# Kernel optimization log

Hardware: AMD Instinct MI355X
Metric: run time of the kernel (lower is better)

## Reference

```python
import jax, jax.numpy as jnp
import numpy as np

N_NODES = 50000
N_EDGES = 800000
DIM_IN = 128
DIM_OUT = 64


def setup_inputs() -> dict:
    key = jax.random.key(0)
    k1, k2, k3, k4 = jax.random.split(key, 4)
    x = jax.random.normal(k1, (N_NODES, DIM_IN), dtype=jnp.float32)
    edge_index = jax.random.randint(k2, (2, N_EDGES), 0, N_NODES, dtype=jnp.int64)
    W = jax.random.normal(k3, (DIM_IN, DIM_OUT), dtype=jnp.float32) / np.sqrt(DIM_IN)
    b = jax.random.normal(k4, (DIM_OUT,), dtype=jnp.float32) * 0.01
    return {"x": x, "edge_index": edge_index, "W": W, "b": b}


def reference(x, edge_index, W, b):
    # Faithful PyG GCNConv: add self-loops, symmetric deg normalization,
    # linear transform then normalized scatter-add aggregation, then bias.
    N = x.shape[0]
    h = x @ W  # [N, dim_out] — transform before propagate (PyG order)

    loops = jnp.arange(N, dtype=edge_index.dtype)
    src = jnp.concatenate([edge_index[0], loops])  # [E+N]
    dst = jnp.concatenate([edge_index[1], loops])  # [E+N]

    ones = jnp.ones(src.shape[0], dtype=h.dtype)
    deg = jax.ops.segment_sum(ones, dst, num_segments=N)  # in-degree incl. self-loop
    dinv = jnp.where(deg > 0, jax.lax.rsqrt(deg), 0.0)
    norm = dinv[src] * dinv[dst]  # [E+N]

    msgs = h[src] * norm[:, None]  # gather + scale
    out = jax.ops.segment_sum(msgs, dst, num_segments=N) + b  # scatter-add
    return jax.nn.log_softmax(out, axis=1)
```

## Files before the change

kernel.cpp:

```cpp
#include <hip/hip_runtime.h>
#include <hip/hip_fp16.h>
#include <cstdint>
#include <cstddef>

#define N_NODES 50000
#define N_EDGES 800000
#define DIM_IN  128
#define DIM_OUT 64

#define B2SHIFT 8
#define B2NODES 256
#define NB2     ((N_NODES + B2NODES - 1) / B2NODES)
#define EB      4096
#define SORTB   ((N_EDGES + EB - 1) / EB)
#define NE4     (N_EDGES / 4)
#define CAPB    4864
#define GROWS   128
#define GEMMB   ((N_NODES + GROWS - 1) / GROWS)
#define GPAD    16
#define NEGRP   ((N_NODES + 31) / 32)

typedef _Float16 f16x8 __attribute__((ext_vector_type(8)));
typedef float    f32x4 __attribute__((ext_vector_type(4)));

__global__ __launch_bounds__(256) void kFG(const int* __restrict__ ei,
                                           int* __restrict__ gcnt,
                                           unsigned* __restrict__ pairs,
                                           const float* __restrict__ x,
                                           const float* __restrict__ W,
                                           __half* __restrict__ h) {
    const int t = threadIdx.x;
    if (blockIdx.x < SORTB) {
        __shared__ int hcnt[B2NODES];
        __shared__ int cur[B2NODES];
        const int blk = blockIdx.x;
        hcnt[t] = 0;
        __syncthreads();
        const int4* src4 = (const int4*)ei;
        const int4* dst4 = (const int4*)(ei + N_EDGES);
        const int g0 = blk * (EB / 4);
#pragma unroll
        for (int it = 0; it < EB / 1024; ++it) {
            const int g = g0 + it * 256 + t;
            if (g < NE4) {
                const int4 d = dst4[g];
                atomicAdd(&hcnt[d.x >> B2SHIFT], 1);
                atomicAdd(&hcnt[d.y >> B2SHIFT], 1);
                atomicAdd(&hcnt[d.z >> B2SHIFT], 1);
                atomicAdd(&hcnt[d.w >> B2SHIFT], 1);
            }
        }
        __syncthreads();
        {
            const int c = hcnt[t];
            const int base = c ? atomicAdd(&gcnt[t * GPAD], c) : 0;
            cur[t] = t * CAPB + base;
        }
        __syncthreads();
#pragma unroll
        for (int it = 0; it < EB / 1024; ++it) {
            const int g = g0 + it * 256 + t;
            if (g < NE4) {
                const int4 sv = src4[g];
                const int4 dv = dst4[g];
                int b, p;
                b = dv.x >> B2SHIFT; p = atomicAdd(&cur[b], 1);
                if (p < b * CAPB + CAPB) pairs[p] = ((unsigned)sv.x << 16) | (unsigned)dv.x;
                b = dv.y >> B2SHIFT; p = atomicAdd(&cur[b], 1);
                if (p < b * CAPB + CAPB) pairs[p] = ((unsigned)sv.y << 16) | (unsigned)dv.y;
                b = dv.z >> B2SHIFT; p = atomicAdd(&cur[b], 1);
                if (p < b * CAPB + CAPB) pairs[p] = ((unsigned)sv.z << 16) | (unsigned)dv.z;
                b = dv.w >> B2SHIFT; p = atomicAdd(&cur[b], 1);
                if (p < b * CAPB + CAPB) pairs[p] = ((unsigned)sv.w << 16) | (unsigned)dv.w;
            }
        }
    } else {
        const int u = blockIdx.x - SORTB;
        const int w = t >> 6;
        const int l = t & 63;
        const int q = l >> 4;
        const int m16 = l & 15;

        f16x8 bf[4][4];
#pragma unroll
        for (int kc = 0; kc < 4; ++kc)
#pragma unroll
            for (int ct = 0; ct < 4; ++ct) {
                const float* wp = W + (size_t)(kc * 32 + q * 8) * DIM_OUT + ct * 16 + m16;
                f16x8 v;
#pragma unroll
                for (int j = 0; j < 8; ++j) v[j] = (_Float16)wp[(size_t)j * DIM_OUT];
                bf[kc][ct] = v;
            }

        const int base = u * GROWS + w * 32;
#pragma unroll
        for (int rt = 0; rt < 2; ++rt) {
            const int m0 = base + rt * 16;
            int mrow = m0 + m16;
            if (mrow >= N_NODES) mrow = N_NODES - 1;

            f16x8 af[4];
#pragma unroll
            for (int kc = 0; kc < 4; ++kc) {
                const float4* xp = (const float4*)(x + (size_t)mrow * DIM_IN + kc * 32 + q * 8);
                const float4 p0 = xp[0], p1 = xp[1];
                f16x8 a;
                a[0] = (_Float16)p0.x; a[1] = (_Float16)p0.y;
                a[2] = (_Float16)p0.z; a[3] = (_Float16)p0.w;
                a[4] = (_Float16)p1.x; a[5] = (_Float16)p1.y;
                a[6] = (_Float16)p1.z; a[7] = (_Float16)p1.w;
                af[kc] = a;
            }

            f32x4 acc[4];
#pragma unroll
            for (int ct = 0; ct < 4; ++ct) acc[ct] = (f32x4){0.f, 0.f, 0.f, 0.f};
#pragma unroll
            for (int kc = 0; kc < 4; ++kc)
#pragma unroll
                for (int ct = 0; ct < 4; ++ct)
                    acc[ct] = __builtin_amdgcn_mfma_f32_16x16x32_f16(af[kc], bf[kc][ct], acc[ct], 0, 0, 0);

#pragma unroll
            for (int reg = 0; reg < 4; ++reg) {
                const int r = m0 + q * 4 + reg;
                if (r < N_NODES) {
#pragma unroll
                    for (int ct = 0; ct < 4; ++ct)
                        h[(size_t)r * DIM_OUT + ct * 16 + m16] = __float2half(acc[ct][reg]);
                }
            }
        }
    }
}

__global__ __launch_bounds__(512) void kSort(const unsigned* __restrict__ pairs,
                                             const int* __restrict__ gcnt,
                                             unsigned short* __restrict__ csr,
                                             int2* __restrict__ nodeoff2,
                                             float* __restrict__ dinv) {
    __shared__ int cnt[B2NODES];
    __shared__ int cur[B2NODES];
    __shared__ int wsum[4];
    __shared__ unsigned short lcsr[CAPB];
    const int b = blockIdx.x, t = threadIdx.x;
    const int eb = b * CAPB;
    const int count = min(gcnt[b * GPAD], CAPB);
    const int ee = eb + count;

    if (t < B2NODES) cnt[t] = 0;
    __syncthreads();

    {
        int i = eb + t;
        for (; i + 1536 < ee; i += 2048) {
            const unsigned p0 = pairs[i];
            const unsigned p1 = pairs[i + 512];
            const unsigned p2 = pairs[i + 1024];
            const unsigned p3 = pairs[i + 1536];
            atomicAdd(&cnt[p0 & (B2NODES - 1)], 1);
            atomicAdd(&cnt[p1 & (B2NODES - 1)], 1);
            atomicAdd(&cnt[p2 & (B2NODES - 1)], 1);
            atomicAdd(&cnt[p3 & (B2NODES - 1)], 1);
        }
        for (; i < ee; i += 512) atomicAdd(&cnt[pairs[i] & (B2NODES - 1)], 1);
    }
    __syncthreads();

    if (t < B2NODES) {
        const int lane = t & 63;
        const int v = cnt[t];
        int xs = v;
#pragma unroll
        for (int off = 1; off < 64; off <<= 1) {
            int y = __shfl_up(xs, off);
            if (lane >= off) xs += y;
        }
        cur[t] = xs;
        if (lane == 63) wsum[t >> 6] = xs;
    }
    __syncthreads();
    if (t == 0) {
        int acc = 0;
#pragma unroll
        for (int w2 = 0; w2 < 4; ++w2) { const int v2 = wsum[w2]; wsum[w2] = acc; acc += v2; }
    }
    __syncthreads();
    if (t < B2NODES) {
        const int v = cnt[t];
        const int excl = cur[t] - v + wsum[t >> 6];
        const int n = (b << B2SHIFT) + t;
        if (n < N_NODES) {
            nodeoff2[n] = make_int2(eb + excl, v);
            dinv[n] = rsqrtf((float)(v + 1));
        }
        cur[t] = excl;
    }
    __syncthreads();

    for (int i = eb + t; i < ee; i += 512) {
        const unsigned p = pairs[i];
        const int q = atomicAdd(&cur[p & (B2NODES - 1)], 1);
        lcsr[q] = (unsigned short)(p >> 16);
    }
    __syncthreads();

    {
        const int cw = (count + 1) >> 1;
        const unsigned* l32 = (const unsigned*)lcsr;
        unsigned* c32 = (unsigned*)(csr + eb);
        for (int i2 = t; i2 < cw; i2 += 512) c32[i2] = l32[i2];
    }
}

__global__ __launch_bounds__(256) void kE_agg(const int2* __restrict__ nodeoff2,
                                              const unsigned short* __restrict__ csr,
                                              const __half* __restrict__ h,
                                              const float* __restrict__ dinv,
                                              const float* __restrict__ bvec,
                                              float* __restrict__ out) {
    const int t = threadIdx.x;
    const int ew = t >> 3, sl = t & 7;
    const int n = blockIdx.x * 32 + ew;
    if (n >= N_NODES) return;
    const f16x8* __restrict__ h8 = (const f16x8*)h;

    const int2 off = nodeoff2[n];
    const int s0 = off.x, s1 = off.x + off.y;
    const float di = rsqrtf((float)(off.y + 1));

    const f16x8 hv = h8[(size_t)n * 8 + sl];
    float a[8];
#pragma unroll
    for (int j = 0; j < 8; ++j) a[j] = (float)hv[j] * di;

    int i = s0;
    for (; i + 8 <= s1; i += 8) {
        int   c[8];
        float d[8];
        f16x8 v[8];
#pragma unroll
        for (int j = 0; j < 8; ++j) c[j] = csr[i + j];
#pragma unroll
        for (int j = 0; j < 8; ++j) d[j] = dinv[c[j]];
#pragma unroll
        for (int j = 0; j < 8; ++j) v[j] = h8[(size_t)c[j] * 8 + sl];
#pragma unroll
        for (int j = 0; j < 8; ++j)
#pragma unroll
            for (int k = 0; k < 8; ++k) a[k] += (float)v[j][k] * d[j];
    }
    for (; i + 4 <= s1; i += 4) {
        const int c0 = csr[i + 0], c1 = csr[i + 1];
        const int c2 = csr[i + 2], c3 = csr[i + 3];
        const float d0 = dinv[c0], d1 = dinv[c1], d2 = dinv[c2], d3 = dinv[c3];
        const f16x8 v0 = h8[(size_t)c0 * 8 + sl];
        const f16x8 v1 = h8[(size_t)c1 * 8 + sl];
        const f16x8 v2 = h8[(size_t)c2 * 8 + sl];
        const f16x8 v3 = h8[(size_t)c3 * 8 + sl];
#pragma unroll
        for (int j = 0; j < 8; ++j)
            a[j] += (float)v0[j] * d0 + (float)v1[j] * d1
                  + (float)v2[j] * d2 + (float)v3[j] * d3;
    }
    for (; i < s1; ++i) {
        const int c = csr[i];
        const float d = dinv[c];
        const f16x8 v0 = h8[(size_t)c * 8 + sl];
#pragma unroll
        for (int j = 0; j < 8; ++j) a[j] += (float)v0[j] * d;
    }

    const float4 b0 = *(const float4*)&bvec[8 * sl];
    const float4 b1 = *(const float4*)&bvec[8 * sl + 4];
    float v[8];
    v[0] = a[0] * di + b0.x; v[1] = a[1] * di + b0.y;
    v[2] = a[2] * di + b0.z; v[3] = a[3] * di + b0.w;
    v[4] = a[4] * di + b1.x; v[5] = a[5] * di + b1.y;
    v[6] = a[6] * di + b1.z; v[7] = a[7] * di + b1.w;

    float m = v[0];
#pragma unroll
    for (int j = 1; j < 8; ++j) m = fmaxf(m, v[j]);
#pragma unroll
    for (int o = 4; o > 0; o >>= 1) m = fmaxf(m, __shfl_xor(m, o));
    float s = 0.f;
#pragma unroll
    for (int j = 0; j < 8; ++j) s += __expf(v[j] - m);
#pragma unroll
    for (int o = 4; o > 0; o >>= 1) s += __shfl_xor(s, o);
    const float ls = m + __logf(s);

    float4 o0, o1;
    o0.x = v[0] - ls; o0.y = v[1] - ls; o0.z = v[2] - ls; o0.w = v[3] - ls;
    o1.x = v[4] - ls; o1.y = v[5] - ls; o1.z = v[6] - ls; o1.w = v[7] - ls;
    *(float4*)&out[(size_t)n * DIM_OUT + 8 * sl]     = o0;
    *(float4*)&out[(size_t)n * DIM_OUT + 8 * sl + 4] = o1;
}

extern "C" void kernel_launch(void* const* d_in, const int* in_sizes, int n_in,
                              void* d_out, int out_size, void* d_ws, size_t ws_size,
                              hipStream_t stream) {
    const float* x  = (const float*)d_in[0];
    const int*   ei = (const int*)d_in[1];
    const float* W  = (const float*)d_in[2];
    const float* b  = (const float*)d_in[3];
    float* out = (float*)d_out;

    char* ws = (char*)d_ws;
    __half*         h        = (__half*)ws;         ws += (size_t)N_NODES * DIM_OUT * sizeof(__half);
    unsigned*       pairs    = (unsigned*)ws;       ws += (size_t)NB2 * CAPB * sizeof(unsigned);
    unsigned short* csr      = (unsigned short*)ws; ws += (size_t)NB2 * CAPB * sizeof(unsigned short);
    int2*           nodeoff2 = (int2*)ws;           ws += (size_t)N_NODES * sizeof(int2);
    float*          dinv     = (float*)ws;          ws += (size_t)N_NODES * sizeof(float);
    int*            gcnt     = (int*)ws;            ws += (size_t)NB2 * GPAD * sizeof(int);

    hipMemsetAsync(gcnt, 0, (size_t)NB2 * GPAD * sizeof(int), stream);
    kFG    <<<SORTB + GEMMB, 256, 0, stream>>>(ei, gcnt, pairs, x, W, h);
    kSort  <<<NB2, 512, 0, stream>>>(pairs, gcnt, csr, nodeoff2, dinv);
    kE_agg <<<NEGRP, 256, 0, stream>>>(nodeoff2, csr, h, dinv, b, out);
}
```

Before: 117.1 us.

## Fuse bucket scatter and per-bucket sort into one kernel via full-edge rescan

Removes the global pairs buffer, the gcnt memset and the separate sort kernel. Each of the 196 bucket blocks now scans the whole destination array, keeps only edges landing in its own bucket in shared memory, then counting-sorts them locally. The GEMM blocks move to 512 threads with 256 rows per block. This saves two launches and one global round trip, but each bucket block re-reads all 3.2MB of destinations, so the sort work grows from O(E) to O(E·buckets) in L2 traffic.

```diff
diff --git a/kernel.cpp b/kernel.cpp
--- a/kernel.cpp
+++ b/kernel.cpp
@@ -11,71 +11,111 @@
 #define B2SHIFT 8
 #define B2NODES 256
 #define NB2     ((N_NODES + B2NODES - 1) / B2NODES)
-#define EB      4096
-#define SORTB   ((N_EDGES + EB - 1) / EB)
 #define NE4     (N_EDGES / 4)
 #define CAPB    4864
-#define GROWS   128
+#define GROWS   256
 #define GEMMB   ((N_NODES + GROWS - 1) / GROWS)
-#define GPAD    16
 #define NEGRP   ((N_NODES + 31) / 32)
 
 typedef _Float16 f16x8 __attribute__((ext_vector_type(8)));
 typedef float    f32x4 __attribute__((ext_vector_type(4)));
 
-__global__ __launch_bounds__(256) void kFG(const int* __restrict__ ei,
-                                           int* __restrict__ gcnt,
-                                           unsigned* __restrict__ pairs,
+__global__ __launch_bounds__(512) void kSG(const int* __restrict__ ei,
                                            const float* __restrict__ x,
                                            const float* __restrict__ W,
-                                           __half* __restrict__ h) {
+                                           __half* __restrict__ h,
+                                           unsigned short* __restrict__ csr,
+                                           int2* __restrict__ nodeoff2,
+                                           float* __restrict__ dinv) {
     const int t = threadIdx.x;
-    if (blockIdx.x < SORTB) {
-        __shared__ int hcnt[B2NODES];
+    if (blockIdx.x < NB2) {
+        __shared__ unsigned cap[CAPB];
+        __shared__ int cnt[B2NODES];
         __shared__ int cur[B2NODES];
-        const int blk = blockIdx.x;
-        hcnt[t] = 0;
-        __syncthreads();
-        const int4* src4 = (const int4*)ei;
-        const int4* dst4 = (const int4*)(ei + N_EDGES);
-        const int g0 = blk * (EB / 4);
-#pragma unroll
-        for (int it = 0; it < EB / 1024; ++it) {
-            const int g = g0 + it * 256 + t;
-            if (g < NE4) {
+        __shared__ int wsum[4];
+        __shared__ int ncap;
+        __shared__ unsigned short lcsr[CAPB];
+        const int b = blockIdx.x;
+        if (t == 0) ncap = 0;
+        if (t < B2NODES) cnt[t] = 0;
+        __syncthreads();
+
+        {
+            const int4* __restrict__ dst4 = (const int4*)(ei + N_EDGES);
+            const int* __restrict__ srcs = ei;
+            for (int g = t; g < NE4; g += 512) {
                 const int4 d = dst4[g];
-                atomicAdd(&hcnt[d.x >> B2SHIFT], 1);
-                atomicAdd(&hcnt[d.y >> B2SHIFT], 1);
-                atomicAdd(&hcnt[d.z >> B2SHIFT], 1);
-                atomicAdd(&hcnt[d.w >> B2SHIFT], 1);
-            }
-        }
-        __syncthreads();
+                if ((d.x >> B2SHIFT) == b) {
+                    const int p = atomicAdd(&ncap, 1);
+                    if (p < CAPB) cap[p] = ((unsigned)srcs[4 * g + 0] << 16) | (unsigned)(d.x & 0xFFFF);
+                }
+                if ((d.y >> B2SHIFT) == b) {
+                    const int p = atomicAdd(&ncap, 1);
+                    if (p < CAPB) cap[p] = ((unsigned)srcs[4 * g + 1] << 16) | (unsigned)(d.y & 0xFFFF);
+                }
+                if ((d.z >> B2SHIFT) == b) {
+                    const int p = atomicAdd(&ncap, 1);
+                    if (p < CAPB) cap[p] = ((unsigned)srcs[4 * g + 2] << 16) | (unsigned)(d.z & 0xFFFF);
+                }
+                if ((d.w >> B2SHIFT) == b) {
+                    const int p = atomicAdd(&ncap, 1);
+                    if (p < CAPB) cap[p] = ((unsigned)srcs[4 * g + 3] << 16) | (unsigned)(d.w & 0xFFFF);
+                }
+            }
+        }
+        __syncthreads();
+        const int total = min(ncap, CAPB);
+
+        for (int i = t; i < total; i += 512)
+            atomicAdd(&cnt[cap[i] & (B2NODES - 1)], 1);
+        __syncthreads();
+
+        if (t < B2NODES) {
+            const int lane = t & 63;
+            const int v = cnt[t];
+            int xs = v;
+#pragma unroll
+            for (int off = 1; off < 64; off <<= 1) {
+                int y = __shfl_up(xs, off);
+                if (lane >= off) xs += y;
+            }
+            cur[t] = xs;
+            if (lane == 63) wsum[t >> 6] = xs;
+        }
+        __syncthreads();
+        if (t == 0) {
+            int acc = 0;
+#pragma unroll
+            for (int w2 = 0; w2 < 4; ++w2) { const int v2 = wsum[w2]; wsum[w2] = acc; acc += v2; }
+        }
+        __syncthreads();
+        if (t < B2NODES) {
+            const int v = cnt[t];
+            const int excl = cur[t] - v + wsum[t >> 6];
+            const int n = (b << B2SHIFT) + t;
+            if (n < N_NODES) {
+                nodeoff2[n] = make_int2(b * CAPB + excl, v);
+                dinv[n] = rsqrtf((float)(v + 1));
+            }
+            cur[t] = excl;
+        }
+        __syncthreads();
+
+        for (int i = t; i < total; i += 512) {
+            const unsigned p = cap[i];
+            const int q = atomicAdd(&cur[p & (B2NODES - 1)], 1);
+            lcsr[q] = (unsigned short)(p >> 16);
+        }
+        __syncthreads();
+
         {
-            const int c = hcnt[t];
-            const int base = c ? atomicAdd(&gcnt[t * GPAD], c) : 0;
-            cur[t] = t * CAPB + base;
-        }
-        __syncthreads();
-#pragma unroll
-        for (int it = 0; it < EB / 1024; ++it) {
-            const int g = g0 + it * 256 + t;
-            if (g < NE4) {
-                const int4 sv = src4[g];
-                const int4 dv = dst4[g];
-                int b, p;
-                b = dv.x >> B2SHIFT; p = atomicAdd(&cur[b], 1);
-                if (p < b * CAPB + CAPB) pairs[p] = ((unsigned)sv.x << 16) | (unsigned)dv.x;
-                b = dv.y >> B2SHIFT; p = atomicAdd(&cur[b], 1);
-                if (p < b * CAPB + CAPB) pairs[p] = ((unsigned)sv.y << 16) | (unsigned)dv.y;
-                b = dv.z >> B2SHIFT; p = atomicAdd(&cur[b], 1);
-                if (p < b * CAPB + CAPB) pairs[p] = ((unsigned)sv.z << 16) | (unsigned)dv.z;
-                b = dv.w >> B2SHIFT; p = atomicAdd(&cur[b], 1);
-                if (p < b * CAPB + CAPB) pairs[p] = ((unsigned)sv.w << 16) | (unsigned)dv.w;
-            }
+            const int cw = (total + 1) >> 1;
+            const unsigned* l32 = (const unsigned*)lcsr;
+            unsigned* c32 = (unsigned*)(csr + b * CAPB);
+            for (int i2 = t; i2 < cw; i2 += 512) c32[i2] = l32[i2];
         }
     } else {
-        const int u = blockIdx.x - SORTB;
+        const int u = blockIdx.x - NB2;
         const int w = t >> 6;
         const int l = t & 63;
         const int q = l >> 4;
@@ -132,85 +172,6 @@
                 }
             }
         }
-    }
-}
-
-__global__ __launch_bounds__(512) void kSort(const unsigned* __restrict__ pairs,
-                                             const int* __restrict__ gcnt,
-                                             unsigned short* __restrict__ csr,
-                                             int2* __restrict__ nodeoff2,
-                                             float* __restrict__ dinv) {
-    __shared__ int cnt[B2NODES];
-    __shared__ int cur[B2NODES];
-    __shared__ int wsum[4];
-    __shared__ unsigned short lcsr[CAPB];
-    const int b = blockIdx.x, t = threadIdx.x;
-    const int eb = b * CAPB;
-    const int count = min(gcnt[b * GPAD], CAPB);
-    const int ee = eb + count;
-
-    if (t < B2NODES) cnt[t] = 0;
-    __syncthreads();
-
-    {
-        int i = eb + t;
-        for (; i + 1536 < ee; i += 2048) {
-            const unsigned p0 = pairs[i];
-            const unsigned p1 = pairs[i + 512];
-            const unsigned p2 = pairs[i + 1024];
-            const unsigned p3 = pairs[i + 1536];
-            atomicAdd(&cnt[p0 & (B2NODES - 1)], 1);
-            atomicAdd(&cnt[p1 & (B2NODES - 1)], 1);
-            atomicAdd(&cnt[p2 & (B2NODES - 1)], 1);
-            atomicAdd(&cnt[p3 & (B2NODES - 1)], 1);
-        }
-        for (; i < ee; i += 512) atomicAdd(&cnt[pairs[i] & (B2NODES - 1)], 1);
-    }
-    __syncthreads();
-
-    if (t < B2NODES) {
-        const int lane = t & 63;
-        const int v = cnt[t];
-        int xs = v;
-#pragma unroll
-        for (int off = 1; off < 64; off <<= 1) {
-            int y = __shfl_up(xs, off);
-            if (lane >= off) xs += y;
-        }
-        cur[t] = xs;
-        if (lane == 63) wsum[t >> 6] = xs;
-    }
-    __syncthreads();
-    if (t == 0) {
-        int acc = 0;
-#pragma unroll
-        for (int w2 = 0; w2 < 4; ++w2) { const int v2 = wsum[w2]; wsum[w2] = acc; acc += v2; }
-    }
-    __syncthreads();
-    if (t < B2NODES) {
-        const int v = cnt[t];
-        const int excl = cur[t] - v + wsum[t >> 6];
-        const int n = (b << B2SHIFT) + t;
-        if (n < N_NODES) {
-            nodeoff2[n] = make_int2(eb + excl, v);
-            dinv[n] = rsqrtf((float)(v + 1));
-        }
-        cur[t] = excl;
-    }
-    __syncthreads();
-
-    for (int i = eb + t; i < ee; i += 512) {
-        const unsigned p = pairs[i];
-        const int q = atomicAdd(&cur[p & (B2NODES - 1)], 1);
-        lcsr[q] = (unsigned short)(p >> 16);
-    }
-    __syncthreads();
-
-    {
-        const int cw = (count + 1) >> 1;
-        const unsigned* l32 = (const unsigned*)lcsr;
-        unsigned* c32 = (unsigned*)(csr + eb);
-        for (int i2 = t; i2 < cw; i2 += 512) c32[i2] = l32[i2];
     }
 }
 
@@ -310,14 +271,10 @@
 
     char* ws = (char*)d_ws;
     __half*         h        = (__half*)ws;         ws += (size_t)N_NODES * DIM_OUT * sizeof(__half);
-    unsigned*       pairs    = (unsigned*)ws;       ws += (size_t)NB2 * CAPB * sizeof(unsigned);
     unsigned short* csr      = (unsigned short*)ws; ws += (size_t)NB2 * CAPB * sizeof(unsigned short);
     int2*           nodeoff2 = (int2*)ws;           ws += (size_t)N_NODES * sizeof(int2);
     float*          dinv     = (float*)ws;          ws += (size_t)N_NODES * sizeof(float);
-    int*            gcnt     = (int*)ws;            ws += (size_t)NB2 * GPAD * sizeof(int);
-
-    hipMemsetAsync(gcnt, 0, (size_t)NB2 * GPAD * sizeof(int), stream);
-    kFG    <<<SORTB + GEMMB, 256, 0, stream>>>(ei, gcnt, pairs, x, W, h);
-    kSort  <<<NB2, 512, 0, stream>>>(pairs, gcnt, csr, nodeoff2, dinv);
+
+    kSG    <<<NB2 + GEMMB, 512, 0, stream>>>(ei, x, W, h, csr, nodeoff2, dinv);
     kE_agg <<<NEGRP, 256, 0, stream>>>(nodeoff2, csr, h, dinv, b, out);
 }
```

Result: slower. 320.4 us (+173.6%).
